# Kernel tuning notes

Hardware: AMD Instinct MI355X
Metric: run time of the kernel (lower is better)

Reference implementation:

```python
import jax, jax.numpy as jnp
import numpy as np

CHEB_K = 3  # matches init_kwargs


def setup_inputs() -> dict:
    key = jax.random.key(0)
    k1, k2, k3, k4 = jax.random.split(key, 4)
    B, N, C_IN, C_OUT, D = 64, 4000, 64, 64, 10
    x = jax.random.normal(k1, (B, N, C_IN), dtype=jnp.float32)
    node_emb = jax.random.normal(k2, (N, D), dtype=jnp.float32)
    weights_pool = jax.random.normal(k3, (D, CHEB_K, C_IN, C_OUT), dtype=jnp.float32) * 0.1
    bias_pool = jax.random.normal(k4, (D, C_OUT), dtype=jnp.float32) * 0.1
    return {"x": x, "node_emb": node_emb, "weights_pool": weights_pool, "bias_pool": bias_pool}


def reference(x, node_emb, weights_pool, bias_pool):
    # adpadj == 'agcrn': adaptive adjacency from node embeddings
    N = node_emb.shape[0]
    supports = jax.nn.softmax(jax.nn.relu(node_emb @ node_emb.T), axis=1)  # [N,N]
    # Chebyshev polynomial basis: T0=I, T1=A, Tk = 2A Tk-1 - Tk-2
    support_set = [jnp.eye(N, dtype=x.dtype), supports]
    for _ in range(2, CHEB_K):
        support_set.append(2.0 * supports @ support_set[-1] - support_set[-2])
    S = jnp.stack(support_set, axis=0)  # [K,N,N]
    # per-node generated weights and bias
    weights = jnp.einsum('nd,dkio->nkio', node_emb, weights_pool)  # [N,K,Cin,Cout]
    bias = node_emb @ bias_pool  # [N,Cout]
    # graph conv: aggregate neighbors for each Chebyshev order, then per-node matmul
    x_g = jnp.einsum('knm,bmc->bnkc', S, x)  # [B,N,K,Cin]
    out = jnp.einsum('bnki,nkio->bno', x_g, weights) + bias  # [B,N,Cout]
    return out
```

## Files before the change

### kernel.cpp

```cpp
#include <hip/hip_runtime.h>

typedef __attribute__((ext_vector_type(8))) __bf16 bf16x8;
typedef __attribute__((ext_vector_type(4))) float f32x4;
typedef __attribute__((ext_vector_type(8))) unsigned short u16x8;
typedef __attribute__((ext_vector_type(4))) unsigned short u16x4;

#define N_NODES 4000
#define LD 4096
#define D_EMB 10
#define NT 64

__device__ __forceinline__ unsigned short f2bf(float f) {
  union { float f; unsigned int u; } v; v.f = f;
  unsigned int r = v.u + 0x7fffu + ((v.u >> 16) & 1u);
  return (unsigned short)(r >> 16);
}
__device__ __forceinline__ float bf2f(unsigned short s) {
  union { unsigned int u; float f; } v; v.u = ((unsigned int)s) << 16;
  return v.f;
}

#define AS1 __attribute__((address_space(1)))
#define AS3 __attribute__((address_space(3)))
__device__ __forceinline__ void gll16(const void* g, void* l) {
  __builtin_amdgcn_global_load_lds((const AS1 void*)g, (AS3 void*)l, 16, 0, 0);
}

__global__ __launch_bounds__(256) void transpose_x_kernel(const float* __restrict__ x,
                                                          unsigned short* __restrict__ Xc) {
  __shared__ float tl[64 * 65];
  const int t = threadIdx.x;
  const int m0 = blockIdx.x * 64;
  const int b = blockIdx.y;
#pragma unroll
  for (int rep = 0; rep < 16; ++rep) {
    int idx = rep * 256 + t;
    int ml = idx >> 6, c = idx & 63;
    int m = m0 + ml;
    tl[ml * 65 + c] = (m < N_NODES) ? x[(b * N_NODES + m) * 64 + c] : 0.f;
  }
  __syncthreads();
  const int c_out = t >> 2, q = t & 3;
  u16x8 v0, v1;
#pragma unroll
  for (int j = 0; j < 8; ++j) v0[j] = f2bf(tl[(q * 16 + j) * 65 + c_out]);
#pragma unroll
  for (int j = 0; j < 8; ++j) v1[j] = f2bf(tl[(q * 16 + 8 + j) * 65 + c_out]);
  unsigned short* dst = Xc + (size_t)(b * 64 + c_out) * LD + m0 + q * 16;
  *(u16x8*)dst = v0;
  *(u16x8*)(dst + 8) = v1;
}

__global__ __launch_bounds__(256) void build_adj_kernel(const float* __restrict__ emb,
                                                        unsigned short* __restrict__ A) {
  __shared__ float e_lds[N_NODES];
  __shared__ float embn[16];
  __shared__ float red[16];
  const int n = blockIdx.x, t = threadIdx.x;
  if (n >= N_NODES) {
    for (int m = t; m < LD; m += 256) A[(size_t)n * LD + m] = 0;
    return;
  }
  if (t < D_EMB) embn[t] = emb[n * D_EMB + t];
  __syncthreads();
  float lsum = 0.f;
  for (int m = t; m < N_NODES; m += 256) {
    float dot = 0.f;
#pragma unroll
    for (int d = 0; d < D_EMB; ++d) dot += embn[d] * emb[m * D_EMB + d];
    float e = __expf(fmaxf(dot, 0.f));
    e_lds[m] = e;
    lsum += e;
  }
#pragma unroll
  for (int off = 32; off > 0; off >>= 1) lsum += __shfl_down(lsum, off, 64);
  const int lane = t & 63, wave = t >> 6;
  if (lane == 0) red[wave] = lsum;
  __syncthreads();
  if (t == 0) red[8] = 1.f / (red[0] + red[1] + red[2] + red[3]);
  __syncthreads();
  const float inv = red[8];
  for (int m = t; m < LD; m += 256) {
    float v = (m < N_NODES) ? e_lds[m] * inv : 0.f;
    A[(size_t)n * LD + m] = f2bf(v);
  }
}

__global__ __launch_bounds__(256) void wpt_kernel(const float* __restrict__ wp,
                                                  unsigned short* __restrict__ wpT) {
  __shared__ float tl[64 * 65];
  const int dk = blockIdx.x;
  const int d = dk / 3, k = dk % 3;
  const float* src = wp + (size_t)dk * 4096;
  const int t = threadIdx.x;
#pragma unroll
  for (int rep = 0; rep < 16; ++rep) {
    int idx = rep * 256 + t;
    tl[(idx >> 6) * 65 + (idx & 63)] = src[idx];
  }
  __syncthreads();
#pragma unroll
  for (int rep = 0; rep < 16; ++rep) {
    int idx = rep * 256 + t;
    int o = idx >> 6, i = idx & 63;
    wpT[(size_t)d * 12288 + o * 192 + k * 64 + i] = f2bf(tl[i * 65 + o]);
  }
}

__global__ __launch_bounds__(256) void wgen_kernel(const float* __restrict__ emb,
                                                   const unsigned short* __restrict__ wpT,
                                                   unsigned short* __restrict__ W_all) {
  __shared__ float el[50 * D_EMB];
  const int t = threadIdx.x;
  const int j = blockIdx.x * 256 + t;
  const int n0 = blockIdx.y * 50;
  for (int idx = t; idx < 50 * D_EMB; idx += 256) el[idx] = emb[n0 * D_EMB + idx];
  __syncthreads();
  float w[D_EMB];
#pragma unroll
  for (int d = 0; d < D_EMB; ++d) w[d] = bf2f(wpT[(size_t)d * 12288 + j]);
  for (int n = 0; n < 50; ++n) {
    float a = 0.f;
#pragma unroll
    for (int d = 0; d < D_EMB; ++d) a += el[n * D_EMB + d] * w[d];
    W_all[(size_t)(n0 + n) * 12288 + j] = f2bf(a);
  }
}

template <bool WRITE_T>
__global__ __launch_bounds__(512, 2) void gemm256_kernel(const unsigned short* __restrict__ Amat,
                                                         const unsigned short* __restrict__ Bmat,
                                                         unsigned short* __restrict__ Cn,
                                                         unsigned short* __restrict__ Ct) {
  __shared__ __align__(128) char smem[131072];
  const int tid = threadIdx.x;
  const int wave = tid >> 6, lane = tid & 63;
  const int wr = wave >> 2, wc = wave & 3;
  const int bm = blockIdx.y * 256, bn = blockIdx.x * 256;
  const int l15 = lane & 15, quad = lane >> 4;
  const int swz = (lane & 7) << 4;
  const int k0 = (quad * 16) ^ swz;
  const int k1 = (64 + quad * 16) ^ swz;

  const char* Ard = smem + (wr * 128 + l15) * 128;
  const char* Brd = smem + 65536 + (wc * 64 + l15) * 128;

  const int u = tid >> 3;
  const int xc = ((tid & 7) ^ (u & 7)) << 3;
  const unsigned short* gA = Amat + (size_t)(bm + u) * LD + xc;
  const unsigned short* gB = Bmat + (size_t)(bn + (u >> 5) * 64 + (u & 31)) * LD + xc;
  char* dA = smem + wave * 1024;
  char* dB = smem + 65536 + (wave >> 2) * 8192 + (wave & 3) * 1024;

#define STAGE_A(P, H, KT) do { \
    gll16(gA + (size_t)((H) * 64) * LD + (KT) * 64,       dA + (P) * 32768 + (H) * 8192); \
    gll16(gA + (size_t)((H) * 64 + 128) * LD + (KT) * 64, dA + (P) * 32768 + (H) * 8192 + 16384); \
  } while (0)
#define STAGE_B(P, H, KT) do { \
    gll16(gB + (size_t)((H) * 32) * LD + (KT) * 64,       dB + (P) * 32768 + (H) * 4096); \
    gll16(gB + (size_t)((H) * 32 + 128) * LD + (KT) * 64, dB + (P) * 32768 + (H) * 4096 + 16384); \
  } while (0)
#define BAR __builtin_amdgcn_s_barrier()
#define LGKM0 asm volatile("s_waitcnt lgkmcnt(0)" ::: "memory")
#define LGKM8 asm volatile("s_waitcnt lgkmcnt(8)" ::: "memory")
#define VM6  asm volatile("s_waitcnt vmcnt(6)" ::: "memory")

  f32x4 acc[8][4] = {};
  bf16x8 a0[4][2], a1[4][2], b0[2][2], b1[2][2];

#define READ_A(DST, MH, P) do { _Pragma("unroll") for (int m = 0; m < 4; ++m) { \
    DST[m][0] = *(const bf16x8*)(Ard + (P) * 32768 + ((MH) * 4 + m) * 2048 + k0); \
    DST[m][1] = *(const bf16x8*)(Ard + (P) * 32768 + ((MH) * 4 + m) * 2048 + k1); } } while (0)
#define READ_B(DST, NH, P) do { _Pragma("unroll") for (int n = 0; n < 2; ++n) { \
    DST[n][0] = *(const bf16x8*)(Brd + (P) * 32768 + ((NH) * 2 + n) * 2048 + k0); \
    DST[n][1] = *(const bf16x8*)(Brd + (P) * 32768 + ((NH) * 2 + n) * 2048 + k1); } } while (0)
#define MFMA_Q(AR, BR, MH, NH) do { _Pragma("unroll") for (int m = 0; m < 4; ++m) \
    _Pragma("unroll") for (int n = 0; n < 2; ++n) { \
      f32x4 c = acc[(MH) * 4 + m][(NH) * 2 + n]; \
      c = __builtin_amdgcn_mfma_f32_16x16x32_bf16(AR[m][0], BR[n][0], c, 0, 0, 0); \
      c = __builtin_amdgcn_mfma_f32_16x16x32_bf16(AR[m][1], BR[n][1], c, 0, 0, 0); \
      acc[(MH) * 4 + m][(NH) * 2 + n] = c; } } while (0)

  STAGE_A(0, 0, 0);
  STAGE_B(0, 0, 0);
  STAGE_B(0, 1, 0);
  STAGE_A(0, 1, 0);
  STAGE_A(1, 0, 1);
  STAGE_B(1, 0, 1);
  STAGE_B(1, 1, 1);
  VM6;
  BAR;

#define TILE(T, P) do { \
    const int kt1 = ((T) + 1 < NT) ? (T) + 1 : 0;  \
    const int kt2 = ((T) + 2 < NT) ? (T) + 2 : 0; \
     \
    READ_A(a0, 0, P); READ_B(b0, 0, P); \
    STAGE_A((P) ^ 1, 1, kt1); \
    LGKM8; \
    BAR; LGKM0; \
    __builtin_amdgcn_s_setprio(1); MFMA_Q(a0, b0, 0, 0); __builtin_amdgcn_s_setprio(0); \
    BAR; \
     \
    READ_B(b1, 1, P); \
    STAGE_A(P, 0, kt2); \
    BAR; LGKM0; \
    __builtin_amdgcn_s_setprio(1); MFMA_Q(a0, b1, 0, 1); __builtin_amdgcn_s_setprio(0); \
    BAR; \
     \
    READ_A(a1, 1, P); \
    STAGE_B(P, 0, kt2); \
    BAR; LGKM0; \
    __builtin_amdgcn_s_setprio(1); MFMA_Q(a1, b0, 1, 0); __builtin_amdgcn_s_setprio(0); \
    BAR; \
     \
    STAGE_B(P, 1, kt2); \
    VM6; \
    BAR; \
    __builtin_amdgcn_s_setprio(1); MFMA_Q(a1, b1, 1, 1); __builtin_amdgcn_s_setprio(0); \
    BAR; \
  } while (0)

#pragma unroll 1
  for (int t = 0; t < NT; t += 2) {
    TILE(t, 0);
    TILE(t + 1, 1);
  }

#pragma unroll
  for (int mt = 0; mt < 8; ++mt)
#pragma unroll
    for (int nt = 0; nt < 4; ++nt) {
      const int row0 = bm + wr * 128 + mt * 16 + quad * 4;
      const int col = bn + wc * 64 + nt * 16 + l15;
#pragma unroll
      for (int r = 0; r < 4; ++r)
        Cn[(size_t)(row0 + r) * LD + col] = f2bf(acc[mt][nt][r]);
    }

  if (WRITE_T) {
    unsigned short* tr = (unsigned short*)smem;
    asm volatile("s_waitcnt vmcnt(0)" ::: "memory");
    __syncthreads();
#pragma unroll
    for (int ch = 0; ch < 2; ++ch) {
      if ((wc >> 1) == ch) {
#pragma unroll
        for (int mt = 0; mt < 8; ++mt)
#pragma unroll
          for (int nt = 0; nt < 4; ++nt) {
            const int coll = (wc & 1) * 64 + nt * 16 + l15;
            const int row0 = wr * 128 + mt * 16 + quad * 4;
#pragma unroll
            for (int r = 0; r < 4; ++r)
              tr[coll * 264 + row0 + r] = f2bf(acc[mt][nt][r]);
          }
      }
      __syncthreads();
      {
        const int coll = tid >> 2, seg = tid & 3;
        const unsigned short* src = tr + coll * 264 + seg * 64;
        unsigned short* dst = Ct + (size_t)(bn + ch * 128 + coll) * LD + bm + seg * 64;
#pragma unroll
        for (int j = 0; j < 8; ++j)
          *(u16x8*)(dst + j * 8) = *(const u16x8*)(src + j * 8);
      }
      __syncthreads();
    }
  } else {
    asm volatile("s_waitcnt vmcnt(0)" ::: "memory");
  }
#undef TILE
#undef MFMA_Q
#undef READ_B
#undef READ_A
#undef VM6
#undef LGKM8
#undef LGKM0
#undef BAR
#undef STAGE_B
#undef STAGE_A
}

#define EST 200
__global__ __launch_bounds__(256) void epilogue_kernel(const float* __restrict__ x,
                                                       const float* __restrict__ emb,
                                                       const unsigned short* __restrict__ W_all,
                                                       const float* __restrict__ bp,
                                                       const unsigned short* __restrict__ Y1,
                                                       const unsigned short* __restrict__ Y2,
                                                       float* __restrict__ out) {
  __shared__ unsigned short Wt[64 * EST];
  __shared__ unsigned short xg[64 * EST];
  __shared__ float embn[16];
  const int n = blockIdx.x, t = threadIdx.x;
  if (t < D_EMB) embn[t] = emb[n * D_EMB + t];

  {
    const int o = t >> 2, sub = t & 3;
    const unsigned short* srcW = W_all + (size_t)n * 12288 + o * 192 + sub * 48;
    unsigned short* dstW = Wt + o * EST + sub * 48;
#pragma unroll
    for (int c = 0; c < 6; ++c)
      *(u16x8*)(dstW + c * 8) = *(const u16x8*)(srcW + c * 8);
  }
  for (int idx = t; idx < 1024; idx += 256) {
    int b = idx >> 4, c4 = (idx & 15) * 4;
    f32x4 v = *(const f32x4*)(x + (size_t)(b * N_NODES + n) * 64 + c4);
    u16x4 s;
#pragma unroll
    for (int j = 0; j < 4; ++j) s[j] = f2bf(v[j]);
    *(u16x4*)(xg + b * EST + c4) = s;
  }
  for (int idx = t; idx < 512; idx += 256) {
    int b = idx >> 3, c8 = (idx & 7) * 8;
    *(u16x8*)(xg + b * EST + 64 + c8) = *(const u16x8*)(Y1 + (size_t)n * LD + b * 64 + c8);
  }
  __syncthreads();
  for (int idx = t; idx < 512; idx += 256) {
    int b = idx >> 3, c8 = (idx & 7) * 8;
    u16x8 y2 = *(const u16x8*)(Y2 + (size_t)n * LD + b * 64 + c8);
    u16x8 r;
#pragma unroll
    for (int j = 0; j < 8; ++j)
      r[j] = f2bf(2.f * bf2f(y2[j]) - bf2f(xg[b * EST + c8 + j]));
    *(u16x8*)(xg + b * EST + 128 + c8) = r;
  }
  __syncthreads();

  const int wave = t >> 6, lane = t & 63, quad = lane >> 4;
  const unsigned short* Apx = xg + (wave * 16 + (lane & 15)) * EST + quad * 8;
  f32x4 acc[4] = {};
#pragma unroll
  for (int step = 0; step < 6; ++step) {
    int koff = step * 32;
    bf16x8 a = *(const bf16x8*)(Apx + koff);
#pragma unroll
    for (int nt = 0; nt < 4; ++nt) {
      bf16x8 bfr = *(const bf16x8*)(Wt + (nt * 16 + (lane & 15)) * EST + quad * 8 + koff);
      acc[nt] = __builtin_amdgcn_mfma_f32_16x16x32_bf16(a, bfr, acc[nt], 0, 0, 0);
    }
  }
  float bias[4];
#pragma unroll
  for (int nt = 0; nt < 4; ++nt) {
    float a = 0.f;
#pragma unroll
    for (int d = 0; d < D_EMB; ++d) a += embn[d] * bp[d * 64 + nt * 16 + (lane & 15)];
    bias[nt] = a;
  }
#pragma unroll
  for (int nt = 0; nt < 4; ++nt)
#pragma unroll
    for (int rr = 0; rr < 4; ++rr) {
      int b_row = wave * 16 + quad * 4 + rr;
      out[(size_t)(b_row * N_NODES + n) * 64 + nt * 16 + (lane & 15)] = acc[nt][rr] + bias[nt];
    }
}

extern "C" void kernel_launch(void* const* d_in, const int* in_sizes, int n_in,
                              void* d_out, int out_size, void* d_ws, size_t ws_size,
                              hipStream_t stream) {
  const float* x   = (const float*)d_in[0];
  const float* emb = (const float*)d_in[1];
  const float* wp  = (const float*)d_in[2];
  const float* bp  = (const float*)d_in[3];
  float* out = (float*)d_out;

  const size_t S = (size_t)LD * LD;
  unsigned short* Y1    = (unsigned short*)d_ws;
  unsigned short* Y2    = Y1 + S;
  unsigned short* Xc    = Y1 + 2 * S;
  unsigned short* Am    = Y1 + 3 * S;
  unsigned short* Y1t   = Y1 + 4 * S;
  unsigned short* wpT   = Xc;
  unsigned short* W_all = Xc + 256 * 1024;

  transpose_x_kernel<<<dim3(64, 64), 256, 0, stream>>>(x, Xc);
  build_adj_kernel<<<LD, 256, 0, stream>>>(emb, Am);
  gemm256_kernel<true ><<<dim3(16, 16), 512, 0, stream>>>(Am, Xc, Y1, Y1t);
  gemm256_kernel<false><<<dim3(16, 16), 512, 0, stream>>>(Am, Y1t, Y2, nullptr);
  wpt_kernel<<<30, 256, 0, stream>>>(wp, wpT);
  wgen_kernel<<<dim3(48, 80), 256, 0, stream>>>(emb, wpT, W_all);
  epilogue_kernel<<<N_NODES, 256, 0, stream>>>(x, emb, W_all, bp, Y1, Y2, out);
}
```

Before: 480.4 us.

## Overlap LDS fragment reads with MFMA via software-pipelined GEMM main loop

Restructures the bf16 GEMM main loop so each phase issues the LDS reads for the next fragment and a global-to-LDS stage, then runs MFMAs on already-loaded registers. The next tile's first A/B fragments are prefetched during the current tile, and a prologue loads them before the loop. Sched barriers pin the ordering, and the waits are reduced to one barrier per phase. This aims to hide LDS and global latency behind matrix math. In exchange it relies on tighter vmcnt accounting, which risks races on buffer reuse.

```diff
diff --git a/kernel.cpp b/kernel.cpp
--- a/kernel.cpp
+++ b/kernel.cpp
@@ -162,8 +162,10 @@
   } while (0)
 #define BAR __builtin_amdgcn_s_barrier()
 #define LGKM0 asm volatile("s_waitcnt lgkmcnt(0)" ::: "memory")
-#define LGKM8 asm volatile("s_waitcnt lgkmcnt(8)" ::: "memory")
-#define VM6  asm volatile("s_waitcnt vmcnt(6)" ::: "memory")
+#define VM8  asm volatile("s_waitcnt vmcnt(8)" ::: "memory")
+#define SB0 __builtin_amdgcn_sched_barrier(0)
+#define SETP1 __builtin_amdgcn_s_setprio(1)
+#define SETP0 __builtin_amdgcn_s_setprio(0)
 
   f32x4 acc[8][4] = {};
   bf16x8 a0[4][2], a1[4][2], b0[2][2], b1[2][2];
@@ -181,50 +183,53 @@
       c = __builtin_amdgcn_mfma_f32_16x16x32_bf16(AR[m][1], BR[n][1], c, 0, 0, 0); \
       acc[(MH) * 4 + m][(NH) * 2 + n] = c; } } while (0)
 
+  STAGE_B(0, 0, 0);
   STAGE_A(0, 0, 0);
-  STAGE_B(0, 0, 0);
+  STAGE_A(0, 1, 0);
   STAGE_B(0, 1, 0);
-  STAGE_A(0, 1, 0);
+  STAGE_B(1, 0, 1);
   STAGE_A(1, 0, 1);
-  STAGE_B(1, 0, 1);
+  STAGE_A(1, 1, 1);
   STAGE_B(1, 1, 1);
-  VM6;
+  VM8;
   BAR;
-
-#define TILE(T, P) do { \
-    const int kt1 = ((T) + 1 < NT) ? (T) + 1 : 0;  \
-    const int kt2 = ((T) + 2 < NT) ? (T) + 2 : 0; \
-     \
-    READ_A(a0, 0, P); READ_B(b0, 0, P); \
-    STAGE_A((P) ^ 1, 1, kt1); \
-    LGKM8; \
-    BAR; LGKM0; \
-    __builtin_amdgcn_s_setprio(1); MFMA_Q(a0, b0, 0, 0); __builtin_amdgcn_s_setprio(0); \
-    BAR; \
+  READ_A(a0, 0, 0);
+  READ_B(b0, 0, 0);
+  LGKM0;
+  BAR;
+
+#define TILE(T, P, Q) do { \
+    const int kt2 = ((T) + 2 < NT) ? (T) + 2 : 0;  \
      \
     READ_B(b1, 1, P); \
-    STAGE_A(P, 0, kt2); \
-    BAR; LGKM0; \
-    __builtin_amdgcn_s_setprio(1); MFMA_Q(a0, b1, 0, 1); __builtin_amdgcn_s_setprio(0); \
-    BAR; \
+    STAGE_B(P, 0, kt2); \
+    SB0; \
+    SETP1; MFMA_Q(a0, b0, 0, 0); SETP0; \
+    LGKM0; BAR; \
      \
     READ_A(a1, 1, P); \
-    STAGE_B(P, 0, kt2); \
-    BAR; LGKM0; \
-    __builtin_amdgcn_s_setprio(1); MFMA_Q(a1, b0, 1, 0); __builtin_amdgcn_s_setprio(0); \
-    BAR; \
+    STAGE_A(P, 0, kt2); \
+    SB0; \
+    SETP1; MFMA_Q(a0, b1, 0, 1); SETP0; \
+    LGKM0; VM8; BAR; \
      \
+    READ_A(a0, 0, Q); \
+    STAGE_A(P, 1, kt2); \
+    SB0; \
+    SETP1; MFMA_Q(a1, b0, 1, 0); SETP0; \
+    LGKM0; BAR; \
+     \
+    READ_B(b0, 0, Q); \
     STAGE_B(P, 1, kt2); \
-    VM6; \
-    BAR; \
-    __builtin_amdgcn_s_setprio(1); MFMA_Q(a1, b1, 1, 1); __builtin_amdgcn_s_setprio(0); \
-    BAR; \
+    SB0; \
+    SETP1; MFMA_Q(a1, b1, 1, 1); SETP0; \
+    LGKM0; VM8; BAR; \
   } while (0)
 
 #pragma unroll 1
   for (int t = 0; t < NT; t += 2) {
-    TILE(t, 0);
-    TILE(t + 1, 1);
+    TILE(t, 0, 1);
+    TILE(t + 1, 1, 0);
   }
 
 #pragma unroll
@@ -274,8 +279,10 @@
 #undef MFMA_Q
 #undef READ_B
 #undef READ_A
-#undef VM6
-#undef LGKM8
+#undef SETP0
+#undef SETP1
+#undef SB0
+#undef VM8
 #undef LGKM0
 #undef BAR
 #undef STAGE_B
```

New measurement: 473.3 us. About the same (-1.5%).
